# Performance work log

Hardware: AMD Instinct MI355X
Metric: run time of the kernel (lower is better)

Reference implementation:

```python
import jax, jax.numpy as jnp
import numpy as np

N = 262144      # total points
B = 128         # scenes (batch segments), 2048 points each
C_IN, C_MID, C_OUT = 256, 256, 512
SIGMA_EPS = 1e-4

def setup_inputs() -> dict:
    key = jax.random.key(0)
    k1, k2, k3, k4, k5 = jax.random.split(key, 5)
    pos = jax.random.normal(k1, (N, 3), dtype=jnp.float32)
    feature = jax.random.normal(k2, (N, C_IN), dtype=jnp.float32)
    batch = jnp.repeat(jnp.arange(B, dtype=jnp.int64), N // B)  # sorted segment ids, no empty segments
    W1 = jax.random.normal(k3, (C_IN + 3, C_MID), dtype=jnp.float32) * 0.02
    b1 = jnp.zeros((C_MID,), dtype=jnp.float32)
    W2 = jax.random.normal(k4, (C_MID, C_OUT), dtype=jnp.float32) * 0.02
    b2 = jnp.zeros((C_OUT,), dtype=jnp.float32)
    noise = jax.random.normal(k5, (B, C_OUT // 2), dtype=jnp.float32)  # reparam eps
    return {"pos": pos, "feature": feature, "batch": batch,
            "W1": W1, "b1": b1, "W2": W2, "b2": b2, "noise": noise}

def reference(pos, feature, batch, W1, b1, W2, b2, noise):
    # scatter_mean: per-scene centroid  [B,3]
    counts = jax.ops.segment_sum(jnp.ones((pos.shape[0],), pos.dtype), batch, num_segments=B)
    pos_center = jax.ops.segment_sum(pos, batch, num_segments=B) / counts[:, None]
    # PointConv with edges (i -> batch[i]): relative position gather
    rel = pos - pos_center[batch]                                  # [N,3]
    msg = jnp.concatenate([feature, rel], axis=1) @ W1 + b1        # [N, C_MID]
    msg = jax.nn.relu(msg)
    agg = jax.ops.segment_max(msg, batch, num_segments=B)          # [B, C_MID] (PointNetConv max aggr)
    out = agg @ W2 + b2                                            # [B, C_OUT]
    mu, sigma_raw = jnp.split(out, 2, axis=1)                      # [B,256] each
    sigma = jax.nn.softplus(sigma_raw) + SIGMA_EPS                 # to_sigma
    z_what_coarse = mu + sigma * noise                             # rsample
    return z_what_coarse
```

## Files before the change

### kernel.cpp

```cpp
#include <hip/hip_runtime.h>
#include <hip/hip_bf16.h>
#include <math.h>

#define PTS_PER 2048

typedef __attribute__((ext_vector_type(8))) short bf16x8;
typedef __attribute__((ext_vector_type(4))) float f32x4;

__device__ __forceinline__ unsigned short f2bf(float f) {
    unsigned u = __float_as_uint(f);
    u += 0x7FFFu + ((u >> 16) & 1u);
    return (unsigned short)(u >> 16);
}

__global__ __launch_bounds__(256) void prep_kernel(
    const float* __restrict__ pos, const float* __restrict__ W1,
    float* __restrict__ center, unsigned short* __restrict__ w1t,
    float* __restrict__ agg) {
    int bid = blockIdx.x, t = threadIdx.x;
    if (bid < 128) {
        __shared__ float red[3 * 256];
        float sx = 0.f, sy = 0.f, sz = 0.f;
        int base = bid * PTS_PER;
        #pragma unroll
        for (int j = 0; j < 8; ++j) {
            int idx = base + j * 256 + t;
            sx += pos[idx * 3 + 0];
            sy += pos[idx * 3 + 1];
            sz += pos[idx * 3 + 2];
        }
        red[t] = sx; red[256 + t] = sy; red[512 + t] = sz;
        __syncthreads();
        for (int s = 128; s > 0; s >>= 1) {
            if (t < s) {
                red[t]       += red[t + s];
                red[256 + t] += red[256 + t + s];
                red[512 + t] += red[512 + t + s];
            }
            __syncthreads();
        }
        if (t == 0) {
            center[bid * 3 + 0] = red[0]   * (1.f / PTS_PER);
            center[bid * 3 + 1] = red[256] * (1.f / PTS_PER);
            center[bid * 3 + 2] = red[512] * (1.f / PTS_PER);
        }
    } else if (bid < 192) {
        int base = ((bid - 128) * 256 + t) * 4;
        int n = base >> 8, k0 = base & 255;
        #pragma unroll
        for (int j = 0; j < 4; ++j)
            w1t[n * 256 + k0 + j] = f2bf(W1[(k0 + j) * 256 + n]);
    } else {
        int idx = ((bid - 192) * 256 + t) * 4;
        *(float4*)(agg + idx) = make_float4(0.f, 0.f, 0.f, 0.f);
    }
}

__global__ __launch_bounds__(256, 3) void main_kernel(
    const float* __restrict__ feature, const float* __restrict__ pos,
    const float* __restrict__ W1, const float* __restrict__ b1,
    const float* __restrict__ center, const unsigned short* __restrict__ w1t,
    float* __restrict__ agg) {
    __shared__ unsigned short sA[64 * 264];
    __shared__ float sRel[64][3];

    int bid = blockIdx.x, t = threadIdx.x;
    int row0 = bid * 64;
    int scene = bid >> 5;

    if (t < 64) {
        int gr = row0 + t;
        sRel[t][0] = pos[gr * 3 + 0] - center[scene * 3 + 0];
        sRel[t][1] = pos[gr * 3 + 1] - center[scene * 3 + 1];
        sRel[t][2] = pos[gr * 3 + 2] - center[scene * 3 + 2];
    }

    const float4* f4 = (const float4*)(feature + (size_t)row0 * 256);
    #pragma unroll
    for (int it = 0; it < 16; ++it) {
        int fidx = it * 256 + t;
        int row = fidx >> 6, c4 = fidx & 63;
        float4 v = f4[fidx];
        ushort4 h;
        h.x = f2bf(v.x); h.y = f2bf(v.y); h.z = f2bf(v.z); h.w = f2bf(v.w);
        *(ushort4*)(sA + row * 264 + c4 * 4) = h;
    }
    __syncthreads();

    int w = t >> 6, lane = t & 63, quad = lane >> 4, lo = lane & 15;

    f32x4 acc[4][4];
    #pragma unroll
    for (int rt = 0; rt < 4; ++rt)
        #pragma unroll
        for (int ct = 0; ct < 4; ++ct)
            acc[rt][ct] = (f32x4){0.f, 0.f, 0.f, 0.f};

    const unsigned short* wbase = w1t + (size_t)(w * 64) * 256;
    #pragma unroll
    for (int k0 = 0; k0 < 256; k0 += 32) {
        int kk = k0 + quad * 8;
        bf16x8 afr[4], bfr[4];
        #pragma unroll
        for (int rt = 0; rt < 4; ++rt)
            afr[rt] = *(const bf16x8*)(sA + (rt * 16 + lo) * 264 + kk);
        #pragma unroll
        for (int ct = 0; ct < 4; ++ct)
            bfr[ct] = *(const bf16x8*)(wbase + (ct * 16 + lo) * 256 + kk);
        #pragma unroll
        for (int rt = 0; rt < 4; ++rt)
            #pragma unroll
            for (int ct = 0; ct < 4; ++ct)
                acc[rt][ct] = __builtin_amdgcn_mfma_f32_16x16x32_bf16(
                    afr[rt], bfr[ct], acc[rt][ct], 0, 0, 0);
    }

    const float* Wp = W1 + 256 * 256;
    #pragma unroll
    for (int ct = 0; ct < 4; ++ct) {
        int col = w * 64 + ct * 16 + lo;
        float wp0 = Wp[col], wp1 = Wp[256 + col], wp2 = Wp[512 + col];
        float m = -3.4e38f;
        #pragma unroll
        for (int rt = 0; rt < 4; ++rt) {
            #pragma unroll
            for (int r = 0; r < 4; ++r) {
                int row = rt * 16 + quad * 4 + r;
                float v = acc[rt][ct][r] + sRel[row][0] * wp0
                        + sRel[row][1] * wp1 + sRel[row][2] * wp2;
                m = fmaxf(m, v);
            }
        }
        m = fmaxf(m, __shfl_xor(m, 16, 64));
        m = fmaxf(m, __shfl_xor(m, 32, 64));
        if (quad == 0) {
            float val = fmaxf(m + b1[col], 0.f);
            atomicMax((unsigned int*)(agg + scene * 256 + col),
                      __float_as_uint(val));
        }
    }
}

__global__ __launch_bounds__(256) void final_kernel(
    const float* __restrict__ agg, const float* __restrict__ W2,
    const float* __restrict__ b2, const float* __restrict__ noise,
    float* __restrict__ out) {
    int s = blockIdx.x, t = threadIdx.x;
    __shared__ float sa[256];
    if (t < 64)
        *(float4*)(sa + t * 4) = *(const float4*)(agg + s * 256 + t * 4);
    __syncthreads();
    float mu = b2[t], sr = b2[256 + t];
    #pragma unroll 4
    for (int k = 0; k < 256; ++k) {
        float a = sa[k];
        mu += a * W2[k * 512 + t];
        sr += a * W2[k * 512 + 256 + t];
    }
    float sp = (sr > 20.f) ? sr : log1pf(expf(sr));
    float sigma = sp + 1e-4f;
    out[s * 256 + t] = mu + sigma * noise[s * 256 + t];
}

extern "C" void kernel_launch(void* const* d_in, const int* in_sizes, int n_in,
                              void* d_out, int out_size, void* d_ws, size_t ws_size,
                              hipStream_t stream) {
    const float* pos     = (const float*)d_in[0];
    const float* feature = (const float*)d_in[1];
    const float* W1      = (const float*)d_in[3];
    const float* b1      = (const float*)d_in[4];
    const float* W2      = (const float*)d_in[5];
    const float* b2      = (const float*)d_in[6];
    const float* noise   = (const float*)d_in[7];
    float* out = (float*)d_out;

    char* ws = (char*)d_ws;
    float* agg            = (float*)ws;
    unsigned short* w1t   = (unsigned short*)(ws + 131072);
    float* center         = (float*)(ws + 262144);

    prep_kernel <<<224, 256, 0, stream>>>(pos, W1, center, w1t, agg);
    main_kernel <<<4096, 256, 0, stream>>>(feature, pos, W1, b1, center, w1t, agg);
    final_kernel<<<128, 256, 0, stream>>>(agg, W2, b2, noise, out);
}
```

Before: 436.5 us.

## Replace atomicMax aggregation with per-block partial maxima reduced in final kernel

Each main-kernel block now writes its per-column max to a partial buffer instead of doing global atomicMax into a zero-initialised aggregate. The final kernel reduces the 32 partials per scene and applies bias and ReLU there, so the agg zeroing in prep is no longer needed. The change also switches to packed hardware bf16 conversion intrinsics and prefetches the first W1 fragment before the feature staging loop. It trades atomic contention for a 4 MB partial buffer write and read, and puts a little more work in the final kernel.

Result: faster. 421.3 us (-3.5%).

```diff
diff --git a/kernel.cpp b/kernel.cpp
--- a/kernel.cpp
+++ b/kernel.cpp
@@ -7,16 +7,21 @@
 typedef __attribute__((ext_vector_type(8))) short bf16x8;
 typedef __attribute__((ext_vector_type(4))) float f32x4;
 
+__device__ __forceinline__ unsigned int pk_bf16(float a, float b) {
+    union { __hip_bfloat162 h; unsigned int u; } cv;
+    cv.h = __float22bfloat162_rn(make_float2(a, b));
+    return cv.u;
+}
+
 __device__ __forceinline__ unsigned short f2bf(float f) {
-    unsigned u = __float_as_uint(f);
-    u += 0x7FFFu + ((u >> 16) & 1u);
-    return (unsigned short)(u >> 16);
+    union { __hip_bfloat16 h; unsigned short u; } cv;
+    cv.h = __float2bfloat16(f);
+    return cv.u;
 }
 
 __global__ __launch_bounds__(256) void prep_kernel(
     const float* __restrict__ pos, const float* __restrict__ W1,
-    float* __restrict__ center, unsigned short* __restrict__ w1t,
-    float* __restrict__ agg) {
+    float* __restrict__ center, unsigned short* __restrict__ w1t) {
     int bid = blockIdx.x, t = threadIdx.x;
     if (bid < 128) {
         __shared__ float red[3 * 256];
@@ -44,23 +49,19 @@
             center[bid * 3 + 1] = red[256] * (1.f / PTS_PER);
             center[bid * 3 + 2] = red[512] * (1.f / PTS_PER);
         }
-    } else if (bid < 192) {
+    } else {
         int base = ((bid - 128) * 256 + t) * 4;
         int n = base >> 8, k0 = base & 255;
         #pragma unroll
         for (int j = 0; j < 4; ++j)
             w1t[n * 256 + k0 + j] = f2bf(W1[(k0 + j) * 256 + n]);
-    } else {
-        int idx = ((bid - 192) * 256 + t) * 4;
-        *(float4*)(agg + idx) = make_float4(0.f, 0.f, 0.f, 0.f);
     }
 }
 
 __global__ __launch_bounds__(256, 3) void main_kernel(
     const float* __restrict__ feature, const float* __restrict__ pos,
-    const float* __restrict__ W1, const float* __restrict__ b1,
-    const float* __restrict__ center, const unsigned short* __restrict__ w1t,
-    float* __restrict__ agg) {
+    const float* __restrict__ W1, const float* __restrict__ center,
+    const unsigned short* __restrict__ w1t, float* __restrict__ partial) {
     __shared__ unsigned short sA[64 * 264];
     __shared__ float sRel[64][3];
 
@@ -75,19 +76,27 @@
         sRel[t][2] = pos[gr * 3 + 2] - center[scene * 3 + 2];
     }
 
+    int w = t >> 6, lane = t & 63, quad = lane >> 4, lo = lane & 15;
+    const unsigned short* wbase = w1t + (size_t)(w * 64) * 256;
+
+    bf16x8 bpre[4];
+    {
+        int kk = quad * 8;
+        #pragma unroll
+        for (int ct = 0; ct < 4; ++ct)
+            bpre[ct] = *(const bf16x8*)(wbase + (ct * 16 + lo) * 256 + kk);
+    }
+
     const float4* f4 = (const float4*)(feature + (size_t)row0 * 256);
     #pragma unroll
     for (int it = 0; it < 16; ++it) {
         int fidx = it * 256 + t;
         int row = fidx >> 6, c4 = fidx & 63;
         float4 v = f4[fidx];
-        ushort4 h;
-        h.x = f2bf(v.x); h.y = f2bf(v.y); h.z = f2bf(v.z); h.w = f2bf(v.w);
-        *(ushort4*)(sA + row * 264 + c4 * 4) = h;
+        uint2 h = make_uint2(pk_bf16(v.x, v.y), pk_bf16(v.z, v.w));
+        *(uint2*)(sA + row * 264 + c4 * 4) = h;
     }
     __syncthreads();
-
-    int w = t >> 6, lane = t & 63, quad = lane >> 4, lo = lane & 15;
 
     f32x4 acc[4][4];
     #pragma unroll
@@ -96,7 +105,6 @@
         for (int ct = 0; ct < 4; ++ct)
             acc[rt][ct] = (f32x4){0.f, 0.f, 0.f, 0.f};
 
-    const unsigned short* wbase = w1t + (size_t)(w * 64) * 256;
     #pragma unroll
     for (int k0 = 0; k0 < 256; k0 += 32) {
         int kk = k0 + quad * 8;
@@ -106,7 +114,8 @@
             afr[rt] = *(const bf16x8*)(sA + (rt * 16 + lo) * 264 + kk);
         #pragma unroll
         for (int ct = 0; ct < 4; ++ct)
-            bfr[ct] = *(const bf16x8*)(wbase + (ct * 16 + lo) * 256 + kk);
+            bfr[ct] = (k0 == 0) ? bpre[ct]
+                    : *(const bf16x8*)(wbase + (ct * 16 + lo) * 256 + kk);
         #pragma unroll
         for (int rt = 0; rt < 4; ++rt)
             #pragma unroll
@@ -133,25 +142,26 @@
         }
         m = fmaxf(m, __shfl_xor(m, 16, 64));
         m = fmaxf(m, __shfl_xor(m, 32, 64));
-        if (quad == 0) {
-            float val = fmaxf(m + b1[col], 0.f);
-            atomicMax((unsigned int*)(agg + scene * 256 + col),
-                      __float_as_uint(val));
-        }
+        if (quad == 0)
+            partial[(size_t)bid * 256 + col] = m;
     }
 }
 
 __global__ __launch_bounds__(256) void final_kernel(
-    const float* __restrict__ agg, const float* __restrict__ W2,
-    const float* __restrict__ b2, const float* __restrict__ noise,
-    float* __restrict__ out) {
+    const float* __restrict__ partial, const float* __restrict__ b1,
+    const float* __restrict__ W2, const float* __restrict__ b2,
+    const float* __restrict__ noise, float* __restrict__ out) {
     int s = blockIdx.x, t = threadIdx.x;
     __shared__ float sa[256];
-    if (t < 64)
-        *(float4*)(sa + t * 4) = *(const float4*)(agg + s * 256 + t * 4);
+    const float* p = partial + (size_t)s * 32 * 256;
+    float m = -3.4e38f;
+    #pragma unroll
+    for (int c = 0; c < 32; ++c)
+        m = fmaxf(m, p[c * 256 + t]);
+    sa[t] = fmaxf(m + b1[t], 0.f);
     __syncthreads();
     float mu = b2[t], sr = b2[256 + t];
-    #pragma unroll 4
+    #pragma unroll 8
     for (int k = 0; k < 256; ++k) {
         float a = sa[k];
         mu += a * W2[k * 512 + t];
@@ -175,11 +185,11 @@
     float* out = (float*)d_out;
 
     char* ws = (char*)d_ws;
-    float* agg            = (float*)ws;
-    unsigned short* w1t   = (unsigned short*)(ws + 131072);
-    float* center         = (float*)(ws + 262144);
+    float* partial        = (float*)ws;
+    unsigned short* w1t   = (unsigned short*)(ws + (4 << 20));
+    float* center         = (float*)(ws + (4 << 20) + 131072);
 
-    prep_kernel <<<224, 256, 0, stream>>>(pos, W1, center, w1t, agg);
-    main_kernel <<<4096, 256, 0, stream>>>(feature, pos, W1, b1, center, w1t, agg);
-    final_kernel<<<128, 256, 0, stream>>>(agg, W2, b2, noise, out);
+    prep_kernel <<<192, 256, 0, stream>>>(pos, W1, center, w1t);
+    main_kernel <<<4096, 256, 0, stream>>>(feature, pos, W1, center, w1t, partial);
+    final_kernel<<<128, 256, 0, stream>>>(partial, b1, W2, b2, noise, out);
 }
```
